# Kernel optimization log

Hardware: AMD Instinct MI355X
Metric: run time of the kernel (lower is better)

## Reference

```python
import jax, jax.numpy as jnp
import numpy as np

NUM_HEADS = 16
NUM_KV_HEADS = 4
HEAD_DIM = 64
HIDDEN = 1024
BATCH, SEQ = 2, 2048
CAUSAL = False


def _rotate_half(x):
    x1, x2 = jnp.split(x, 2, axis=-1)
    return jnp.concatenate([-x2, x1], axis=-1)


def setup_inputs() -> dict:
    key = jax.random.key(0)
    k1, k2, k3 = jax.random.split(key, 3)
    hidden_states = jax.random.normal(k1, (BATCH, SEQ, HIDDEN), dtype=jnp.float32)
    # realistic rotary tables
    inv_freq = 1.0 / (10000.0 ** (np.arange(0, HEAD_DIM, 2, dtype=np.float32) / HEAD_DIM))
    t = np.arange(SEQ, dtype=np.float32)
    freqs = np.outer(t, inv_freq)                      # [S, D/2]
    emb = np.concatenate([freqs, freqs], axis=-1)      # [S, D]
    cos = jnp.asarray(np.cos(emb), dtype=jnp.float32)
    sin = jnp.asarray(np.sin(emb), dtype=jnp.float32)
    qkv_out = (NUM_HEADS + 2 * NUM_KV_HEADS) * HEAD_DIM
    w_qkv = jax.random.normal(k2, (qkv_out, HIDDEN), dtype=jnp.float32) * (HIDDEN ** -0.5)
    w_o = jax.random.normal(k3, (HIDDEN, NUM_HEADS * HEAD_DIM), dtype=jnp.float32) * ((NUM_HEADS * HEAD_DIM) ** -0.5)
    return {"hidden_states": hidden_states, "cos": cos, "sin": sin, "w_qkv": w_qkv, "w_o": w_o}


def reference(hidden_states, cos, sin, w_qkv, w_o):
    b, s, _ = hidden_states.shape
    qkv = jnp.einsum('bsh,oh->bso', hidden_states, w_qkv)
    qkv = qkv.reshape(b, s, NUM_HEADS + 2 * NUM_KV_HEADS, HEAD_DIM)
    q = qkv[:, :, :NUM_HEADS]                                    # [b,s,Hq,d]
    k = qkv[:, :, NUM_HEADS:NUM_HEADS + NUM_KV_HEADS]            # [b,s,Hkv,d]
    v = qkv[:, :, NUM_HEADS + NUM_KV_HEADS:]                     # [b,s,Hkv,d]
    # RoPE (HF style): broadcast cos/sin [s,d] over batch and heads
    c = cos[None, :, None, :]
    sn = sin[None, :, None, :]
    q = q * c + _rotate_half(q) * sn
    k = k * c + _rotate_half(k) * sn
    # GQA: repeat kv heads to match q heads
    rep = NUM_HEADS // NUM_KV_HEADS
    k = jnp.repeat(k, rep, axis=2)
    v = jnp.repeat(v, rep, axis=2)
    scale = HEAD_DIM ** -0.5
    scores = jnp.einsum('bqhd,bkhd->bhqk', q, k) * scale
    if CAUSAL:
        mask = jnp.tril(jnp.ones((s, s), dtype=bool))
        scores = jnp.where(mask[None, None], scores, jnp.finfo(scores.dtype).min)
    probs = jax.nn.softmax(scores, axis=-1)
    attn = jnp.einsum('bhqk,bkhd->bqhd', probs, v)
    attn = attn.reshape(b, s, NUM_HEADS * HEAD_DIM)
    return jnp.einsum('bso,ho->bsh', attn, w_o)
```

## Files before the change

### kernel.cpp

```cpp
#include <hip/hip_runtime.h>
#include <hip/hip_bf16.h>

typedef unsigned short u16;
typedef unsigned int u32;
typedef __attribute__((ext_vector_type(8))) short short8;
typedef __attribute__((ext_vector_type(4))) float f32x4;
typedef __attribute__((ext_vector_type(16))) float f32x16;
typedef __attribute__((ext_vector_type(4))) u32 u32x4;

__device__ __forceinline__ u16 f2b(float f) {
    __hip_bfloat16 h = __float2bfloat16(f);
    return *reinterpret_cast<u16*>(&h);
}
__device__ __forceinline__ float b2f(u16 u) {
    __hip_bfloat16 h;
    *reinterpret_cast<u16*>(&h) = u;
    return __bfloat162float(h);
}
__device__ __forceinline__ u32 cvtpk(float lo, float hi_) {
    u32 r;
    asm("v_cvt_pk_bf16_f32 %0, %1, %2" : "=v"(r) : "v"(lo), "v"(hi_));
    return r;
}
__device__ __forceinline__ void gload16(const void* g, void* l) {
    __builtin_amdgcn_global_load_lds(
        (const __attribute__((address_space(1))) unsigned int*)g,
        (__attribute__((address_space(3))) unsigned int*)l, 16, 0, 0);
}

__global__ void convert_kernel(const float* __restrict__ X, const float* __restrict__ W1,
                               const float* __restrict__ W2,
                               u16* __restrict__ Xb, u16* __restrict__ W1b, u16* __restrict__ W2b) {
    int idx = blockIdx.x * 256 + threadIdx.x;
    const float* src; u16* dst; int off;
    if (idx < 1048576)        { src = X;  dst = Xb;  off = idx; }
    else if (idx < 1441792)   { src = W1; dst = W1b; off = idx - 1048576; }
    else                      { src = W2; dst = W2b; off = idx - 1441792; }
    float4 v = reinterpret_cast<const float4*>(src)[off];
    ushort4 o;
    o.x = f2b(v.x); o.y = f2b(v.y); o.z = f2b(v.z); o.w = f2b(v.w);
    reinterpret_cast<ushort4*>(dst)[off] = o;
}

template <typename OUT>
__global__ __launch_bounds__(256) void gemm_bt(const u16* __restrict__ A, const u16* __restrict__ B,
                                               OUT* __restrict__ C, int M, int N, int K) {
    __shared__ u16 As[128 * 32];
    __shared__ u16 Bs[128 * 32];
    const int tid = threadIdx.x;
    const int lane = tid & 63, wave = tid >> 6;
    const int wm = wave >> 1, wn = wave & 1;
    const int row16 = lane & 15, kgrp = lane >> 4;
    const int bm = blockIdx.x, bn = blockIdx.y;

    f32x4 acc[4][4];
#pragma unroll
    for (int i = 0; i < 4; ++i)
#pragma unroll
        for (int j = 0; j < 4; ++j) acc[i][j] = {0.f, 0.f, 0.f, 0.f};

    for (int kt = 0; kt < K; kt += 32) {
        __syncthreads();
#pragma unroll
        for (int it = 0; it < 2; ++it) {
            int chunk = it * 256 + tid;
            int row = chunk >> 2, c = chunk & 3;
            int cs = c ^ ((row >> 1) & 3);
            gload16(A + (size_t)(bm * 128 + row) * K + kt + cs * 8, &As[chunk * 8]);
            gload16(B + (size_t)(bn * 128 + row) * K + kt + cs * 8, &Bs[chunk * 8]);
        }
        __syncthreads();
        short8 af[4], bfr[4];
#pragma unroll
        for (int mf = 0; mf < 4; ++mf) {
            int r = wm * 64 + mf * 16 + row16;
            af[mf] = *(const short8*)&As[r * 32 + (kgrp ^ ((r >> 1) & 3)) * 8];
        }
#pragma unroll
        for (int nf = 0; nf < 4; ++nf) {
            int r = wn * 64 + nf * 16 + row16;
            bfr[nf] = *(const short8*)&Bs[r * 32 + (kgrp ^ ((r >> 1) & 3)) * 8];
        }
#pragma unroll
        for (int mf = 0; mf < 4; ++mf)
#pragma unroll
            for (int nf = 0; nf < 4; ++nf)
                acc[mf][nf] = __builtin_amdgcn_mfma_f32_16x16x32_bf16(af[mf], bfr[nf], acc[mf][nf], 0, 0, 0);
    }
#pragma unroll
    for (int mf = 0; mf < 4; ++mf)
#pragma unroll
        for (int r = 0; r < 4; ++r) {
            int row = bm * 128 + wm * 64 + mf * 16 + kgrp * 4 + r;
#pragma unroll
            for (int nf = 0; nf < 4; ++nf) {
                int col = bn * 128 + wn * 64 + nf * 16 + row16;
                float v = acc[mf][nf][r];
                if constexpr (sizeof(OUT) == 2) C[(size_t)row * N + col] = f2b(v);
                else                            C[(size_t)row * N + col] = v;
            }
        }
}

__global__ void rope_kernel(const u16* __restrict__ qkv, const float* __restrict__ cosb,
                            const float* __restrict__ sinb, u16* __restrict__ Qa,
                            u16* __restrict__ Ka) {
    int idx = blockIdx.x * 256 + threadIdx.x;
    if (idx < 2097152) {
        int d = idx & 31, h = (idx >> 5) & 15, m = idx >> 9;
        int s = m & 2047, b = m >> 11;
        const u16* src = qkv + (size_t)m * 1536 + h * 64 + d;
        float q1 = b2f(src[0]), q2 = b2f(src[32]);
        float c = cosb[s * 64 + d], sn = sinb[s * 64 + d];
        u16* dst = Qa + ((size_t)(b * 16 + h) * 2048 + s) * 64 + d;
        dst[0]  = f2b((q1 * c - q2 * sn) * 0.125f);
        dst[32] = f2b((q2 * c + q1 * sn) * 0.125f);
    } else {
        int t = idx - 2097152;
        int d = t & 31, kh = (t >> 5) & 3, m = t >> 7;
        int s = m & 2047, b = m >> 11;
        const u16* src = qkv + (size_t)m * 1536 + (16 + kh) * 64 + d;
        float q1 = b2f(src[0]), q2 = b2f(src[32]);
        float c = cosb[s * 64 + d], sn = sinb[s * 64 + d];
        u16* dst = Ka + ((size_t)(b * 4 + kh) * 2048 + s) * 64 + d;
        dst[0]  = f2b(q1 * c - q2 * sn);
        dst[32] = f2b(q2 * c + q1 * sn);
    }
}

__global__ __launch_bounds__(256) void vtrans_kernel(const u16* __restrict__ qkv, u16* __restrict__ Vt) {
    __shared__ u16 T[64 * 71];
    const int tid = threadIdx.x;
    const int sblk = blockIdx.x, kh = blockIdx.y, b = blockIdx.z;
    const u16* src = qkv + (size_t)(b * 2048 + sblk * 64) * 1536 + 1280 + kh * 64;
#pragma unroll
    for (int it = 0; it < 2; ++it) {
        int u = it * 256 + tid;
        int s = u >> 3, c = u & 7;
        short8 v = *(const short8*)(src + (size_t)s * 1536 + c * 8);
#pragma unroll
        for (int i = 0; i < 8; ++i)
            T[(c * 8 + i) * 71 + s] = (u16)v[i];
    }
    __syncthreads();
    u16* dst = Vt + (size_t)(b * 4 + kh) * 64 * 2048 + sblk * 64;
#pragma unroll
    for (int it = 0; it < 2; ++it) {
        int u = it * 256 + tid;
        int d = u >> 3, s0 = (u & 7) * 8;
        short8 o;
#pragma unroll
        for (int i = 0; i < 8; ++i) o[i] = (short)T[d * 71 + s0 + i];
        *(short8*)(dst + (size_t)d * 2048 + s0) = o;
    }
}

__global__ __launch_bounds__(256) void attn_kernel(const u16* __restrict__ Qa,
                                                   const u16* __restrict__ Ka,
                                                   const u16* __restrict__ Vt,
                                                   u16* __restrict__ Ob) {
    __shared__ u16 Ks[64 * 64];
    __shared__ u16 Vs[64 * 64];
    const int tid = threadIdx.x, lane = tid & 63, wave = tid >> 6;
    const int q32 = lane & 31, hi = lane >> 5;
    const int qt = blockIdx.x, h = blockIdx.y, b = blockIdx.z;
    const int kh = h >> 2;
    const u16* Qp = Qa + ((size_t)(b * 16 + h) * 2048 + qt * 128 + wave * 32) * 64;
    const u16* Kp = Ka + (size_t)(b * 4 + kh) * 2048 * 64;
    const u16* Vp = Vt + (size_t)(b * 4 + kh) * 64 * 2048;

    short8 qf[4];
#pragma unroll
    for (int dt = 0; dt < 4; ++dt)
        qf[dt] = *(const short8*)(Qp + q32 * 64 + dt * 16 + hi * 8);

    f32x16 oacc[2];
#pragma unroll
    for (int i = 0; i < 2; ++i)
#pragma unroll
        for (int r = 0; r < 16; ++r) oacc[i][r] = 0.f;
    float lpart = 0.f;

    for (int kvt = 0; kvt < 32; ++kvt) {
        __syncthreads();
#pragma unroll
        for (int it = 0; it < 2; ++it) {
            int chunk = it * 256 + tid;
            int row = chunk >> 3, c = chunk & 7;
            gload16(Kp + (size_t)(kvt * 64 + row) * 64 + ((c ^ (row & 7)) * 8), &Ks[chunk * 8]);
        }
#pragma unroll
        for (int it = 0; it < 2; ++it) {
            int chunk = it * 256 + tid;
            int row = chunk >> 3, c = chunk & 7;
            gload16(Vp + (size_t)row * 2048 + kvt * 64 + ((c ^ (row & 7)) * 8), &Vs[chunk * 8]);
        }
        __syncthreads();

        f32x16 S[2];
#pragma unroll
        for (int i = 0; i < 2; ++i)
#pragma unroll
            for (int r = 0; r < 16; ++r) S[i][r] = 0.f;
#pragma unroll
        for (int kt2 = 0; kt2 < 2; ++kt2) {
            int krow = kt2 * 32 + q32;
#pragma unroll
            for (int dt = 0; dt < 4; ++dt) {
                short8 kf = *(const short8*)&Ks[(krow * 8 + ((dt * 2 + hi) ^ (krow & 7))) * 8];
                S[kt2] = __builtin_amdgcn_mfma_f32_32x32x16_bf16(kf, qf[dt], S[kt2], 0, 0, 0);
            }
        }

#pragma unroll
        for (int kt2 = 0; kt2 < 2; ++kt2)
#pragma unroll
            for (int r = 0; r < 16; ++r) {
                float p = __expf(S[kt2][r]);
                S[kt2][r] = p;
                lpart += p;
            }

#pragma unroll
        for (int kc = 0; kc < 4; ++kc) {
            const int kt2 = kc >> 1, R = (kc & 1) * 8;
            u32 a0 = cvtpk(S[kt2][R + 0], S[kt2][R + 1]);
            u32 b0 = cvtpk(S[kt2][R + 4], S[kt2][R + 5]);
            asm("v_permlane32_swap_b32 %0, %1" : "+v"(a0), "+v"(b0));
            u32 a1 = cvtpk(S[kt2][R + 2], S[kt2][R + 3]);
            u32 b1 = cvtpk(S[kt2][R + 6], S[kt2][R + 7]);
            asm("v_permlane32_swap_b32 %0, %1" : "+v"(a1), "+v"(b1));
            u32x4 pw; pw[0] = a0; pw[1] = a1; pw[2] = b0; pw[3] = b1;
            short8 pf = __builtin_bit_cast(short8, pw);
#pragma unroll
            for (int dt2 = 0; dt2 < 2; ++dt2) {
                int vrow = dt2 * 32 + q32;
                short8 vf = *(const short8*)&Vs[(vrow * 8 + ((kc * 2 + hi) ^ (vrow & 7))) * 8];
                oacc[dt2] = __builtin_amdgcn_mfma_f32_32x32x16_bf16(vf, pf, oacc[dt2], 0, 0, 0);
            }
        }
    }

    float l = lpart + __shfl_xor(lpart, 32);
    float inv = 1.f / l;
    const size_t mbase = ((size_t)(b * 2048 + qt * 128 + wave * 32 + q32)) * 1024 + h * 64;
#pragma unroll
    for (int dt2 = 0; dt2 < 2; ++dt2)
#pragma unroll
        for (int rq = 0; rq < 4; ++rq) {
            ushort4 o;
            o.x = f2b(oacc[dt2][rq * 4 + 0] * inv);
            o.y = f2b(oacc[dt2][rq * 4 + 1] * inv);
            o.z = f2b(oacc[dt2][rq * 4 + 2] * inv);
            o.w = f2b(oacc[dt2][rq * 4 + 3] * inv);
            *(ushort4*)&Ob[mbase + dt2 * 32 + rq * 8 + hi * 4] = o;
        }
}

extern "C" void kernel_launch(void* const* d_in, const int* in_sizes, int n_in,
                              void* d_out, int out_size, void* d_ws, size_t ws_size,
                              hipStream_t stream) {
    const float* X    = (const float*)d_in[0];
    const float* cosb = (const float*)d_in[1];
    const float* sinb = (const float*)d_in[2];
    const float* Wqkv = (const float*)d_in[3];
    const float* Wo   = (const float*)d_in[4];
    float* out = (float*)d_out;
    char* ws = (char*)d_ws;

    u16* Xbf    = (u16*)(ws);
    u16* Wqkvbf = (u16*)(ws + 8388608);
    u16* Wobf   = (u16*)(ws + 11534336);
    u16* QKV    = (u16*)(ws + 13631488);
    u16* Qa     = (u16*)(ws + 26214400);
    u16* Ka     = (u16*)(ws + 34603008);
    u16* Vt     = (u16*)(ws + 36700160);
    u16* attnb  = Xbf;

    convert_kernel<<<6656, 256, 0, stream>>>(X, Wqkv, Wo, Xbf, Wqkvbf, Wobf);
    gemm_bt<u16><<<dim3(32, 12), 256, 0, stream>>>(Xbf, Wqkvbf, QKV, 4096, 1536, 1024);
    rope_kernel<<<10240, 256, 0, stream>>>(QKV, cosb, sinb, Qa, Ka);
    vtrans_kernel<<<dim3(32, 4, 2), 256, 0, stream>>>(QKV, Vt);
    attn_kernel<<<dim3(16, 16, 2), 256, 0, stream>>>(Qa, Ka, Vt, attnb);
    gemm_bt<float><<<dim3(32, 8), 256, 0, stream>>>(attnb, Wobf, out, 4096, 1024, 1024);
}
```

Before: 191.3 us.

## Double-buffer GEMM and attention LDS tiles, shrink GEMM M-tile, use exp2 softmax

Adds double-buffered LDS staging to both the GEMM and the attention kernel, so the next tile's global-to-LDS load overlaps the current tile's MFMA work, with one barrier per iteration. Halves the GEMM M tile to 64 rows, doubling the grid for better CU occupancy. Folds log2(e) into the Q scale so softmax can use raw v_exp_f32, and splits the row-sum accumulator into two chains. Adds s_setprio around the MFMA sections. The trade-offs are more LDS per block and lower per-block data reuse in the GEMM.

```diff
diff --git a/kernel.cpp b/kernel.cpp
--- a/kernel.cpp
+++ b/kernel.cpp
@@ -20,6 +20,11 @@
 __device__ __forceinline__ u32 cvtpk(float lo, float hi_) {
     u32 r;
     asm("v_cvt_pk_bf16_f32 %0, %1, %2" : "=v"(r) : "v"(lo), "v"(hi_));
+    return r;
+}
+__device__ __forceinline__ float fexp2(float x) {
+    float r;
+    asm("v_exp_f32 %0, %1" : "=v"(r) : "v"(x));
     return r;
 }
 __device__ __forceinline__ void gload16(const void* g, void* l) {
@@ -45,53 +50,66 @@
 template <typename OUT>
 __global__ __launch_bounds__(256) void gemm_bt(const u16* __restrict__ A, const u16* __restrict__ B,
                                                OUT* __restrict__ C, int M, int N, int K) {
-    __shared__ u16 As[128 * 32];
-    __shared__ u16 Bs[128 * 32];
+    __shared__ u16 As[2][64 * 32];
+    __shared__ u16 Bs[2][128 * 32];
     const int tid = threadIdx.x;
     const int lane = tid & 63, wave = tid >> 6;
     const int wm = wave >> 1, wn = wave & 1;
     const int row16 = lane & 15, kgrp = lane >> 4;
     const int bm = blockIdx.x, bn = blockIdx.y;
-
-    f32x4 acc[4][4];
-#pragma unroll
-    for (int i = 0; i < 4; ++i)
+    const int nk = K >> 5;
+    const u16* Abase = A + (size_t)bm * 64 * K;
+    const u16* Bbase = B + (size_t)bn * 128 * K;
+
+    f32x4 acc[2][4];
+#pragma unroll
+    for (int i = 0; i < 2; ++i)
 #pragma unroll
         for (int j = 0; j < 4; ++j) acc[i][j] = {0.f, 0.f, 0.f, 0.f};
 
-    for (int kt = 0; kt < K; kt += 32) {
-        __syncthreads();
+    auto stage = [&](int buf, int kt) {
+        {
+            int row = tid >> 2, c = tid & 3;
+            int cs = c ^ ((row >> 1) & 3);
+            gload16(Abase + (size_t)row * K + kt * 32 + cs * 8, &As[buf][tid * 8]);
+        }
 #pragma unroll
         for (int it = 0; it < 2; ++it) {
             int chunk = it * 256 + tid;
             int row = chunk >> 2, c = chunk & 3;
             int cs = c ^ ((row >> 1) & 3);
-            gload16(A + (size_t)(bm * 128 + row) * K + kt + cs * 8, &As[chunk * 8]);
-            gload16(B + (size_t)(bn * 128 + row) * K + kt + cs * 8, &Bs[chunk * 8]);
-        }
-        __syncthreads();
-        short8 af[4], bfr[4];
-#pragma unroll
-        for (int mf = 0; mf < 4; ++mf) {
-            int r = wm * 64 + mf * 16 + row16;
-            af[mf] = *(const short8*)&As[r * 32 + (kgrp ^ ((r >> 1) & 3)) * 8];
+            gload16(Bbase + (size_t)row * K + kt * 32 + cs * 8, &Bs[buf][chunk * 8]);
+        }
+    };
+
+    stage(0, 0);
+    __syncthreads();
+    for (int kt = 0; kt < nk; ++kt) {
+        int cur = kt & 1;
+        if (kt + 1 < nk) stage(cur ^ 1, kt + 1);
+        short8 af[2], bfr[4];
+#pragma unroll
+        for (int mf = 0; mf < 2; ++mf) {
+            int r = wm * 32 + mf * 16 + row16;
+            af[mf] = *(const short8*)&As[cur][r * 32 + (kgrp ^ ((r >> 1) & 3)) * 8];
         }
 #pragma unroll
         for (int nf = 0; nf < 4; ++nf) {
             int r = wn * 64 + nf * 16 + row16;
-            bfr[nf] = *(const short8*)&Bs[r * 32 + (kgrp ^ ((r >> 1) & 3)) * 8];
-        }
-#pragma unroll
-        for (int mf = 0; mf < 4; ++mf)
+            bfr[nf] = *(const short8*)&Bs[cur][r * 32 + (kgrp ^ ((r >> 1) & 3)) * 8];
+        }
+#pragma unroll
+        for (int mf = 0; mf < 2; ++mf)
 #pragma unroll
             for (int nf = 0; nf < 4; ++nf)
                 acc[mf][nf] = __builtin_amdgcn_mfma_f32_16x16x32_bf16(af[mf], bfr[nf], acc[mf][nf], 0, 0, 0);
-    }
-#pragma unroll
-    for (int mf = 0; mf < 4; ++mf)
+        __syncthreads();
+    }
+#pragma unroll
+    for (int mf = 0; mf < 2; ++mf)
 #pragma unroll
         for (int r = 0; r < 4; ++r) {
-            int row = bm * 128 + wm * 64 + mf * 16 + kgrp * 4 + r;
+            int row = bm * 64 + wm * 32 + mf * 16 + kgrp * 4 + r;
 #pragma unroll
             for (int nf = 0; nf < 4; ++nf) {
                 int col = bn * 128 + wn * 64 + nf * 16 + row16;
@@ -113,8 +131,8 @@
         float q1 = b2f(src[0]), q2 = b2f(src[32]);
         float c = cosb[s * 64 + d], sn = sinb[s * 64 + d];
         u16* dst = Qa + ((size_t)(b * 16 + h) * 2048 + s) * 64 + d;
-        dst[0]  = f2b((q1 * c - q2 * sn) * 0.125f);
-        dst[32] = f2b((q2 * c + q1 * sn) * 0.125f);
+        dst[0]  = f2b((q1 * c - q2 * sn) * 0.18033688f);
+        dst[32] = f2b((q2 * c + q1 * sn) * 0.18033688f);
     } else {
         int t = idx - 2097152;
         int d = t & 31, kh = (t >> 5) & 3, m = t >> 7;
@@ -159,8 +177,8 @@
                                                    const u16* __restrict__ Ka,
                                                    const u16* __restrict__ Vt,
                                                    u16* __restrict__ Ob) {
-    __shared__ u16 Ks[64 * 64];
-    __shared__ u16 Vs[64 * 64];
+    __shared__ u16 Ks[2][64 * 64];
+    __shared__ u16 Vs[2][64 * 64];
     const int tid = threadIdx.x, lane = tid & 63, wave = tid >> 6;
     const int q32 = lane & 31, hi = lane >> 5;
     const int qt = blockIdx.x, h = blockIdx.y, b = blockIdx.z;
@@ -179,48 +197,57 @@
     for (int i = 0; i < 2; ++i)
 #pragma unroll
         for (int r = 0; r < 16; ++r) oacc[i][r] = 0.f;
-    float lpart = 0.f;
-
-    for (int kvt = 0; kvt < 32; ++kvt) {
-        __syncthreads();
+    float lpx = 0.f, lpy = 0.f;
+
+    auto stageKV = [&](int buf, int kvt) {
 #pragma unroll
         for (int it = 0; it < 2; ++it) {
             int chunk = it * 256 + tid;
             int row = chunk >> 3, c = chunk & 7;
-            gload16(Kp + (size_t)(kvt * 64 + row) * 64 + ((c ^ (row & 7)) * 8), &Ks[chunk * 8]);
+            gload16(Kp + (size_t)(kvt * 64 + row) * 64 + ((c ^ (row & 7)) * 8), &Ks[buf][chunk * 8]);
         }
 #pragma unroll
         for (int it = 0; it < 2; ++it) {
             int chunk = it * 256 + tid;
             int row = chunk >> 3, c = chunk & 7;
-            gload16(Vp + (size_t)row * 2048 + kvt * 64 + ((c ^ (row & 7)) * 8), &Vs[chunk * 8]);
-        }
-        __syncthreads();
+            gload16(Vp + (size_t)row * 2048 + kvt * 64 + ((c ^ (row & 7)) * 8), &Vs[buf][chunk * 8]);
+        }
+    };
+
+    stageKV(0, 0);
+    __syncthreads();
+    for (int kvt = 0; kvt < 32; ++kvt) {
+        const int cur = kvt & 1;
+        if (kvt + 1 < 32) stageKV(cur ^ 1, kvt + 1);
 
         f32x16 S[2];
 #pragma unroll
         for (int i = 0; i < 2; ++i)
 #pragma unroll
             for (int r = 0; r < 16; ++r) S[i][r] = 0.f;
+        __builtin_amdgcn_s_setprio(1);
 #pragma unroll
         for (int kt2 = 0; kt2 < 2; ++kt2) {
             int krow = kt2 * 32 + q32;
 #pragma unroll
             for (int dt = 0; dt < 4; ++dt) {
-                short8 kf = *(const short8*)&Ks[(krow * 8 + ((dt * 2 + hi) ^ (krow & 7))) * 8];
+                short8 kf = *(const short8*)&Ks[cur][(krow * 8 + ((dt * 2 + hi) ^ (krow & 7))) * 8];
                 S[kt2] = __builtin_amdgcn_mfma_f32_32x32x16_bf16(kf, qf[dt], S[kt2], 0, 0, 0);
             }
         }
+        __builtin_amdgcn_s_setprio(0);
 
 #pragma unroll
         for (int kt2 = 0; kt2 < 2; ++kt2)
 #pragma unroll
-            for (int r = 0; r < 16; ++r) {
-                float p = __expf(S[kt2][r]);
-                S[kt2][r] = p;
-                lpart += p;
+            for (int r = 0; r < 16; r += 2) {
+                float p0 = fexp2(S[kt2][r]);
+                float p1 = fexp2(S[kt2][r + 1]);
+                S[kt2][r] = p0; S[kt2][r + 1] = p1;
+                lpx += p0; lpy += p1;
             }
 
+        __builtin_amdgcn_s_setprio(1);
 #pragma unroll
         for (int kc = 0; kc < 4; ++kc) {
             const int kt2 = kc >> 1, R = (kc & 1) * 8;
@@ -235,12 +262,15 @@
 #pragma unroll
             for (int dt2 = 0; dt2 < 2; ++dt2) {
                 int vrow = dt2 * 32 + q32;
-                short8 vf = *(const short8*)&Vs[(vrow * 8 + ((kc * 2 + hi) ^ (vrow & 7))) * 8];
+                short8 vf = *(const short8*)&Vs[cur][(vrow * 8 + ((kc * 2 + hi) ^ (vrow & 7))) * 8];
                 oacc[dt2] = __builtin_amdgcn_mfma_f32_32x32x16_bf16(vf, pf, oacc[dt2], 0, 0, 0);
             }
         }
-    }
-
+        __builtin_amdgcn_s_setprio(0);
+        __syncthreads();
+    }
+
+    float lpart = lpx + lpy;
     float l = lpart + __shfl_xor(lpart, 32);
     float inv = 1.f / l;
     const size_t mbase = ((size_t)(b * 2048 + qt * 128 + wave * 32 + q32)) * 1024 + h * 64;
@@ -278,9 +308,9 @@
     u16* attnb  = Xbf;
 
     convert_kernel<<<6656, 256, 0, stream>>>(X, Wqkv, Wo, Xbf, Wqkvbf, Wobf);
-    gemm_bt<u16><<<dim3(32, 12), 256, 0, stream>>>(Xbf, Wqkvbf, QKV, 4096, 1536, 1024);
+    gemm_bt<u16><<<dim3(64, 12), 256, 0, stream>>>(Xbf, Wqkvbf, QKV, 4096, 1536, 1024);
     rope_kernel<<<10240, 256, 0, stream>>>(QKV, cosb, sinb, Qa, Ka);
     vtrans_kernel<<<dim3(32, 4, 2), 256, 0, stream>>>(QKV, Vt);
     attn_kernel<<<dim3(16, 16, 2), 256, 0, stream>>>(Qa, Ka, Vt, attnb);
-    gemm_bt<float><<<dim3(32, 8), 256, 0, stream>>>(attnb, Wobf, out, 4096, 1024, 1024);
-}
+    gemm_bt<float><<<dim3(64, 8), 256, 0, stream>>>(attnb, Wobf, out, 4096, 1024, 1024);
+}
```

New measurement: 179.7 us. 1.06x faster.
